# Optimization experiments

Measured on AMD Instinct MI355X. Metric: run time of the kernel, lower is better.

Reference implementation:

```python
import jax, jax.numpy as jnp
import numpy as np
from jax import lax

TAU = 1.0
SIGMAS = (1.0, 1.0, 1.0)
SIGMA_CUTOFF = 2.0
SCALE_FACTORS = (0.5, 1.0)
ITERATIONS = (4, 4)
EPS = 1e-6


def _grid(shape):
    # identity sampling grid in voxel coordinates, (3, D, H, W)
    return jnp.stack(jnp.meshgrid(*[jnp.arange(s, dtype=jnp.float32) for s in shape], indexing='ij'), axis=0)


def warp(vol, flow):
    # vol (B,C,D,H,W), flow (B,3,D,H,W) voxel-space displacements; trilinear, zeros padding
    g = _grid(vol.shape[2:])
    def one_b(v, f):
        coords = g + f  # (3,D,H,W)
        def one_c(ch):
            return jax.scipy.ndimage.map_coordinates(ch, [coords[0], coords[1], coords[2]], order=1, mode='constant', cval=0.0)
        return jax.vmap(one_c)(v)
    return jax.vmap(one_b)(vol, flow)


def gaussian_smooth(x, sigmas=SIGMAS):
    # separable depthwise Gaussian, kernel radius = ceil(sigma_cutoff * sigma)
    C = x.shape[1]
    for axis, sigma in enumerate(sigmas):
        r = int(np.ceil(SIGMA_CUTOFF * sigma))
        t = jnp.arange(-r, r + 1, dtype=x.dtype)
        k = jnp.exp(-0.5 * (t / sigma) ** 2)
        k = k / k.sum()
        kshape = [1, 1, 1, 1, 1]
        kshape[2 + axis] = k.size
        w = jnp.broadcast_to(k.reshape(kshape), (C, 1) + tuple(kshape[2:]))
        x = lax.conv_general_dilated(x, w, (1, 1, 1), 'SAME', feature_group_count=C,
                                     dimension_numbers=('NCDHW', 'OIDHW', 'NCDHW'))
    return x


def _gradient(x, axis):
    # np.gradient style: central diff interior, one-sided at edges, unit spacing
    lo = lax.slice_in_dim(x, 1, 2, axis=axis) - lax.slice_in_dim(x, 0, 1, axis=axis)
    mid = (lax.slice_in_dim(x, 2, None, axis=axis) - lax.slice_in_dim(x, 0, -2, axis=axis)) * 0.5
    hi = lax.slice_in_dim(x, -1, None, axis=axis) - lax.slice_in_dim(x, -2, -1, axis=axis)
    return jnp.concatenate([lo, mid, hi], axis=axis)


def demon_forces(moving, fixed):
    # active demons: gradient of (warped) moving image, (B,1,D,H,W) -> (B,3,D,H,W)
    m = moving[:, 0]
    grads = jnp.stack([_gradient(m, 1), _gradient(m, 2), _gradient(m, 3)], axis=1)
    diff = moving - fixed  # (B,1,D,H,W)
    denom = jnp.sum(grads ** 2, axis=1, keepdims=True) + diff ** 2
    return grads * diff / (denom + EPS)


def resize_tri(x, shape):
    return jax.image.resize(x, x.shape[:2] + tuple(shape), method='trilinear')


def match_vf(vf, shape):
    if tuple(vf.shape[2:]) == tuple(shape):
        return vf
    old = vf.shape[2:]
    out = resize_tri(vf, shape)
    scale = jnp.array([s1 / s2 for s1, s2 in zip(shape, old)], dtype=vf.dtype).reshape(1, 3, 1, 1, 1)
    return out * scale


def run_level(vf, img_s, mask_s, cond_s, iters):
    def body(i, carry):
        vf, _ = carry
        warped = warp(cond_s, vf)
        f = demon_forces(warped, img_s)
        vf = vf - TAU * (f * mask_s)
        vf = gaussian_smooth(vf)
        return (vf, warped)
    return lax.fori_loop(0, iters, body, (vf, jnp.zeros_like(cond_s)))


def conv3d(x, w, b=None):
    y = lax.conv_general_dilated(x, w, (1, 1, 1), 'SAME', dimension_numbers=('NCDHW', 'OIDHW', 'NCDHW'))
    return y if b is None else y + b[None, :, None, None, None]


def instance_norm(x, eps=1e-5):
    m = x.mean(axis=(2, 3, 4), keepdims=True)
    v = x.var(axis=(2, 3, 4), keepdims=True)
    return (x - m) * lax.rsqrt(v + eps)


def mish(x):
    return x * jnp.tanh(jax.nn.softplus(x))


def setup_inputs() -> dict:
    key = jax.random.key(0)
    ks = jax.random.split(key, 8)
    S = (1, 1, 96, 96, 96)
    image = jax.random.normal(ks[0], S, dtype=jnp.float32)
    conditional = jax.random.normal(ks[1], S, dtype=jnp.float32)
    mask = jnp.ones(S, dtype=jnp.float32)
    w1 = jax.random.normal(ks[2], (32, 5, 3, 3, 3), dtype=jnp.float32) * 0.05
    w2 = jax.random.normal(ks[3], (64, 32, 3, 3, 3), dtype=jnp.float32) * 0.05
    w3 = jax.random.normal(ks[4], (32, 64, 3, 3, 3), dtype=jnp.float32) * 0.05
    w4 = jax.random.normal(ks[5], (3, 32, 3, 3, 3), dtype=jnp.float32) * 0.05
    b4 = jnp.zeros((3,), dtype=jnp.float32)
    return {"image": image, "mask": mask, "conditional": conditional,
            "w1": w1, "w2": w2, "w3": w3, "w4": w4, "b4": b4}


def reference(image, mask, conditional, w1, w2, w3, w4, b4):
    full_shape = image.shape[2:]
    vf = None
    warped = None
    for sf, iters in zip(SCALE_FACTORS, ITERATIONS):
        shp = tuple(int(s * sf) for s in full_shape)
        img_s = resize_tri(image, shp)
        mask_s = jax.image.resize(mask, mask.shape[:2] + shp, method='nearest')
        cond_s = resize_tri(conditional, shp)
        if vf is None:
            vf = jnp.zeros((image.shape[0], 3) + shp, image.dtype)
        else:
            vf = match_vf(vf, shp)
        vf, warped = run_level(vf, img_s, mask_s, cond_s, iters)
    # correction network on full-resolution level outputs
    masked_image = image * mask
    stacked = jnp.concatenate([vf, masked_image, warped], axis=1)  # (B,5,D,H,W)
    h = mish(instance_norm(conv3d(stacked, w1)))
    h = mish(instance_norm(conv3d(h, w2)))
    h = mish(instance_norm(conv3d(h, w3)))
    corr = conv3d(h, w4, b4)
    cvf = gaussian_smooth(vf + corr)
    vf_full = match_vf(vf, full_shape)
    cvf_full = match_vf(cvf, full_shape)
    corrected_warped = warp(conditional, cvf_full)
    warped_full = warp(conditional, vf_full)
    return (corrected_warped, warped_full, cvf_full, vf_full)
```

## Files before the change

### kernel.cpp

```cpp
#include <hip/hip_runtime.h>
#include <math.h>

typedef unsigned short ushort_t;
typedef __attribute__((ext_vector_type(8))) short bf16x8;
typedef __attribute__((ext_vector_type(4))) float f32x4;

constexpr int V96 = 96 * 96 * 96;
constexpr int V48 = 48 * 48 * 48;
constexpr int V98 = 98 * 98 * 98;

__device__ __constant__ float GK[5] = {
    0.05448868454964294f, 0.24420134240717082f, 0.40261994608637245f,
    0.24420134240717082f, 0.05448868454964294f };

__device__ __forceinline__ float bf2f(ushort_t u) {
    return __uint_as_float(((unsigned)u) << 16);
}
__device__ __forceinline__ ushort_t f2bf(float f) {
    unsigned x = __float_as_uint(f);
    x += 0x7fffu + ((x >> 16) & 1u);
    return (ushort_t)(x >> 16);
}
__device__ __forceinline__ bool is_bf16(const unsigned* mrw) {
    return mrw[0] == 0x3F803F80u;
}
__device__ __forceinline__ float ld_in(const void* p, int i, bool bf) {
    return bf ? bf2f(((const ushort_t*)p)[i]) : ((const float*)p)[i];
}

constexpr size_t OFF_IMG32 = 0;
constexpr size_t OFF_MSK32 = OFF_IMG32 + V96;
constexpr size_t OFF_COND32 = OFF_MSK32 + V96;
constexpr size_t OFF_VF96 = OFF_COND32 + V96;
constexpr size_t OFF_WTS = OFF_VF96 + 3 * (size_t)V96;
constexpr size_t OFF_ST = OFF_WTS + 117760;
constexpr size_t OFF_PK1 = OFF_ST + 256;
constexpr size_t OFF_PK2 = OFF_PK1 + 3584;
constexpr size_t OFF_PK3 = OFF_PK2 + 27648;
constexpr size_t OFF_PK4 = OFF_PK3 + 27648;
constexpr size_t OFF_B = OFF_PK4 + 6912;
constexpr size_t BSZF = 32 * (size_t)V98 / 2;
constexpr size_t OFF_C = OFF_B + BSZF;
constexpr size_t CSZF = 64 * (size_t)V98;
constexpr size_t WS_FLOATS = OFF_C + CSZF / 2;

constexpr size_t WOB = 117504;

template<int S>
__device__ __forceinline__ void decomp(int r, int& z, int& y, int& x) {
    z = r / (S * S); int r2 = r - z * S * S; y = r2 / S; x = r2 - y * S;
}

__global__ void cvt_in_k(const void* __restrict__ in, float* __restrict__ out, int n,
                         const unsigned* __restrict__ mrw) {
    int i = blockIdx.x * 256 + threadIdx.x;
    if (i >= n) return;
    out[i] = ld_in(in, i, is_bf16(mrw));
}
__global__ void cvt3_k(const void* __restrict__ a, const void* __restrict__ b,
                       const void* __restrict__ c, float* __restrict__ oa,
                       float* __restrict__ ob, float* __restrict__ oc,
                       const unsigned* __restrict__ mrw) {
    int i = blockIdx.x * 256 + threadIdx.x;
    if (i >= V96) return;
    bool bf = is_bf16(mrw);
    oa[i] = ld_in(a, i, bf);
    ob[i] = ld_in(b, i, bf);
    oc[i] = ld_in(c, i, bf);
}
__global__ void store_out_k(const float* __restrict__ in, void* __restrict__ out,
                            size_t off, int n, const unsigned* __restrict__ mrw) {
    int i = blockIdx.x * 256 + threadIdx.x;
    if (i >= n) return;
    if (is_bf16(mrw)) ((ushort_t*)out)[off + i] = f2bf(in[i]);
    else              ((float*)out)[off + i] = in[i];
}
__global__ void add4_k(const float* __restrict__ a, const float* __restrict__ b,
                       float* __restrict__ o, int n4) {
    int i = blockIdx.x * 256 + threadIdx.x;
    if (i >= n4) return;
    float4 A = ((const float4*)a)[i], B = ((const float4*)b)[i];
    float4 O = {A.x + B.x, A.y + B.y, A.z + B.z, A.w + B.w};
    ((float4*)o)[i] = O;
}

template<int C>
__global__ void zero_pad_k(ushort_t* __restrict__ buf) {
    int v = blockIdx.x * 256 + threadIdx.x;
    if (v >= V98) return;
    int z = v / (98 * 98); int r = v - z * 98 * 98; int y = r / 98; int x = r - y * 98;
    if (z != 0 && z != 97 && y != 0 && y != 97 && x != 0 && x != 97) return;
    bf16x8 zv = {};
    bf16x8* p = (bf16x8*)(buf + (size_t)v * C);
#pragma unroll
    for (int c = 0; c < C / 8; ++c) p[c] = zv;
}

__global__ void pack1_k(const void* __restrict__ w, ushort_t* __restrict__ pk,
                        const unsigned* __restrict__ mrw) {
    int i = blockIdx.x * 256 + threadIdx.x;
    if (i >= 7168) return;
    bool bf = is_bf16(mrw);
    int j = i & 7, n = (i >> 3) & 15, ng = (i >> 7) & 1, tq = i >> 8;
    int co = ng * 16 + n;
    float v = (tq < 27 && j < 5) ? ld_in(w, (co * 5 + j) * 27 + tq, bf) : 0.f;
    pk[i] = f2bf(v);
}
__global__ void pack2_k(const void* __restrict__ w, ushort_t* __restrict__ pk,
                        const unsigned* __restrict__ mrw) {
    int i = blockIdx.x * 256 + threadIdx.x;
    if (i >= 55296) return;
    bool bf = is_bf16(mrw);
    int j = i & 7, n = (i >> 3) & 15, q = (i >> 7) & 3, ng = (i >> 9) & 3, t = i >> 11;
    int co = ng * 16 + n, ci = q * 8 + j;
    pk[i] = f2bf(ld_in(w, (co * 32 + ci) * 27 + t, bf));
}
__global__ void pack3_k(const void* __restrict__ w, ushort_t* __restrict__ pk,
                        const unsigned* __restrict__ mrw) {
    int i = blockIdx.x * 256 + threadIdx.x;
    if (i >= 55296) return;
    bool bf = is_bf16(mrw);
    int j = i & 7, n = (i >> 3) & 15, q = (i >> 7) & 3, ng = (i >> 9) & 1, kb = (i >> 10) & 1, t = i >> 11;
    int co = ng * 16 + n, ci = kb * 32 + q * 8 + j;
    pk[i] = f2bf(ld_in(w, (co * 64 + ci) * 27 + t, bf));
}
__global__ void pack4_k(const void* __restrict__ w, ushort_t* __restrict__ pk,
                        const unsigned* __restrict__ mrw) {
    int i = blockIdx.x * 256 + threadIdx.x;
    if (i >= 13824) return;
    bool bf = is_bf16(mrw);
    int j = i & 7, m = (i >> 3) & 15, q = (i >> 7) & 3, t = i >> 9;
    int ci = q * 8 + j;
    float v = (m < 3) ? ld_in(w, (m * 32 + ci) * 27 + t, bf) : 0.f;
    pk[i] = f2bf(v);
}

__device__ __forceinline__ int ds_wt(int i, float w[4]) {
    int j0 = 2 * i - 1;
    w[0] = 0.25f; w[1] = 0.75f; w[2] = 0.75f; w[3] = 0.25f;
    float s = 0.f;
#pragma unroll
    for (int t = 0; t < 4; ++t) { int j = j0 + t; if (j < 0 || j > 95) w[t] = 0.f; s += w[t]; }
    float inv = 1.f / s;
#pragma unroll
    for (int t = 0; t < 4; ++t) w[t] *= inv;
    return j0;
}

__global__ void down_tri_k(const float* __restrict__ in, float* __restrict__ out) {
    int idx = blockIdx.x * 256 + threadIdx.x;
    if (idx >= V48) return;
    int z, y, x; decomp<48>(idx, z, y, x);
    float wz[4], wy[4], wx[4];
    int z0 = ds_wt(z, wz), y0 = ds_wt(y, wy), x0 = ds_wt(x, wx);
    float acc = 0.f;
#pragma unroll
    for (int a = 0; a < 4; ++a) {
        int zz = z0 + a; zz = zz < 0 ? 0 : (zz > 95 ? 95 : zz);
#pragma unroll
        for (int b = 0; b < 4; ++b) {
            int yy = y0 + b; yy = yy < 0 ? 0 : (yy > 95 ? 95 : yy);
            float wzy = wz[a] * wy[b];
#pragma unroll
            for (int c = 0; c < 4; ++c) {
                int xx = x0 + c; xx = xx < 0 ? 0 : (xx > 95 ? 95 : xx);
                acc = fmaf(wzy * wx[c], in[(zz * 96 + yy) * 96 + xx], acc);
            }
        }
    }
    out[idx] = acc;
}

__global__ void down_near_k(const float* __restrict__ in, float* __restrict__ out) {
    int idx = blockIdx.x * 256 + threadIdx.x;
    if (idx >= V48) return;
    int z, y, x; decomp<48>(idx, z, y, x);
    out[idx] = in[((2 * z + 1) * 96 + (2 * y + 1)) * 96 + (2 * x + 1)];
}

__device__ __forceinline__ void up_c(int i, int& i0, float& t) {
    float s = 0.5f * (float)i - 0.25f;
    s = fminf(fmaxf(s, 0.f), 47.f);
    int ii = (int)s; if (ii > 46) ii = 46;
    i0 = ii; t = s - (float)ii;
}

__global__ void up_vf_k(const float* __restrict__ in, float* __restrict__ out) {
    int idx = blockIdx.x * 256 + threadIdx.x;
    if (idx >= 3 * V96) return;
    int c = idx / V96; int r = idx - c * V96;
    int z, y, x; decomp<96>(r, z, y, x);
    int z0, y0, x0; float tz, ty, tx;
    up_c(z, z0, tz); up_c(y, y0, ty); up_c(x, x0, tx);
    const float* p = in + (size_t)c * V48;
    float acc = 0.f;
#pragma unroll
    for (int a = 0; a < 2; ++a)
#pragma unroll
        for (int b = 0; b < 2; ++b)
#pragma unroll
            for (int d = 0; d < 2; ++d) {
                float w = (a ? tz : 1.f - tz) * (b ? ty : 1.f - ty) * (d ? tx : 1.f - tx);
                acc = fmaf(w, p[((z0 + a) * 48 + (y0 + b)) * 48 + (x0 + d)], acc);
            }
    out[idx] = 2.f * acc;
}

template<int S>
__global__ void warp_k(const float* __restrict__ vol, const float* __restrict__ flow,
                       float* __restrict__ out) {
    constexpr int S3 = S * S * S;
    int idx = blockIdx.x * 256 + threadIdx.x;
    if (idx >= S3) return;
    int z, y, x; decomp<S>(idx, z, y, x);
    float cz = (float)z + flow[idx];
    float cy = (float)y + flow[S3 + idx];
    float cx = (float)x + flow[2 * S3 + idx];
    float fz = floorf(cz), fy = floorf(cy), fx = floorf(cx);
    int iz = (int)fz, iy = (int)fy, ix = (int)fx;
    float tz = cz - fz, ty = cy - fy, tx = cx - fx;
    float acc = 0.f;
#pragma unroll
    for (int a = 0; a < 2; ++a)
#pragma unroll
        for (int b = 0; b < 2; ++b)
#pragma unroll
            for (int c = 0; c < 2; ++c) {
                int zz = iz + a, yy = iy + b, xx = ix + c;
                float w = (a ? tz : 1.f - tz) * (b ? ty : 1.f - ty) * (c ? tx : 1.f - tx);
                bool ok = ((unsigned)zz < (unsigned)S) && ((unsigned)yy < (unsigned)S) &&
                          ((unsigned)xx < (unsigned)S);
                float v = ok ? vol[(zz * S + yy) * S + xx] : 0.f;
                acc = fmaf(w, v, acc);
            }
    out[idx] = acc;
}

__global__ void warp_out_k(const float* __restrict__ vol, const float* __restrict__ flow,
                           void* __restrict__ out, size_t off,
                           const unsigned* __restrict__ mrw) {
    constexpr int S = 96, S3 = V96;
    int idx = blockIdx.x * 256 + threadIdx.x;
    if (idx >= S3) return;
    int z, y, x; decomp<S>(idx, z, y, x);
    float cz = (float)z + flow[idx];
    float cy = (float)y + flow[S3 + idx];
    float cx = (float)x + flow[2 * S3 + idx];
    float fz = floorf(cz), fy = floorf(cy), fx = floorf(cx);
    int iz = (int)fz, iy = (int)fy, ix = (int)fx;
    float tz = cz - fz, ty = cy - fy, tx = cx - fx;
    float acc = 0.f;
#pragma unroll
    for (int a = 0; a < 2; ++a)
#pragma unroll
        for (int b = 0; b < 2; ++b)
#pragma unroll
            for (int c = 0; c < 2; ++c) {
                int zz = iz + a, yy = iy + b, xx = ix + c;
                float w = (a ? tz : 1.f - tz) * (b ? ty : 1.f - ty) * (c ? tx : 1.f - tx);
                bool ok = ((unsigned)zz < (unsigned)S) && ((unsigned)yy < (unsigned)S) &&
                          ((unsigned)xx < (unsigned)S);
                float v = ok ? vol[(zz * S + yy) * S + xx] : 0.f;
                acc = fmaf(w, v, acc);
            }
    if (is_bf16(mrw)) ((ushort_t*)out)[off + idx] = f2bf(acc);
    else              ((float*)out)[off + idx] = acc;
}

template<int S>
__global__ void demon4_k(const float* __restrict__ wv, const float* __restrict__ fx_,
                         const float* __restrict__ msk, const float* __restrict__ vin,
                         float* __restrict__ vout) {
    constexpr int S3 = S * S * S;
    int u = blockIdx.x * 256 + threadIdx.x;
    if (u >= S3 / 4) return;
    int idx = u * 4;
    int z, y, x0; decomp<S>(idx, z, y, x0);
    float w[12];
    *(float4*)(w + 4) = *(const float4*)(wv + idx);
    if (x0 > 0) *(float4*)(w + 0) = *(const float4*)(wv + idx - 4);
    else { w[0] = w[1] = w[2] = w[3] = 0.f; }
    if (x0 < S - 4) *(float4*)(w + 8) = *(const float4*)(wv + idx + 4);
    else { w[8] = w[9] = w[10] = w[11] = 0.f; }
    float zp[4], zm[4], yp[4], ym[4];
    float sz = (z == 0 || z == S - 1) ? 1.f : 0.5f;
    float sy = (y == 0 || y == S - 1) ? 1.f : 0.5f;
    if (z > 0) *(float4*)zm = *(const float4*)(wv + idx - S * S);
    else { zm[0] = w[4]; zm[1] = w[5]; zm[2] = w[6]; zm[3] = w[7]; }
    if (z < S - 1) *(float4*)zp = *(const float4*)(wv + idx + S * S);
    else { zp[0] = w[4]; zp[1] = w[5]; zp[2] = w[6]; zp[3] = w[7]; }
    if (y > 0) *(float4*)ym = *(const float4*)(wv + idx - S);
    else { ym[0] = w[4]; ym[1] = w[5]; ym[2] = w[6]; ym[3] = w[7]; }
    if (y < S - 1) *(float4*)yp = *(const float4*)(wv + idx + S);
    else { yp[0] = w[4]; yp[1] = w[5]; yp[2] = w[6]; yp[3] = w[7]; }
    float fx4[4], mk4[4], v0[4], v1[4], v2[4], o0[4], o1[4], o2[4];
    *(float4*)fx4 = *(const float4*)(fx_ + idx);
    *(float4*)mk4 = *(const float4*)(msk + idx);
    *(float4*)v0 = *(const float4*)(vin + idx);
    *(float4*)v1 = *(const float4*)(vin + S3 + idx);
    *(float4*)v2 = *(const float4*)(vin + 2 * S3 + idx);
#pragma unroll
    for (int j = 0; j < 4; ++j) {
        int x = x0 + j;
        float m = w[4 + j];
        float gz = sz * (zp[j] - zm[j]);
        float gy = sy * (yp[j] - ym[j]);
        float gx = (x == 0) ? (w[j + 5] - w[j + 4])
                 : (x == S - 1) ? (w[j + 4] - w[j + 3])
                 : 0.5f * (w[j + 5] - w[j + 3]);
        float diff = m - fx4[j];
        float denom = gz * gz + gy * gy + gx * gx + diff * diff + 1e-6f;
        float r = diff / denom;
        float mk = mk4[j] * r;
        o0[j] = v0[j] - gz * mk;
        o1[j] = v1[j] - gy * mk;
        o2[j] = v2[j] - gx * mk;
    }
    *(float4*)(vout + idx) = *(float4*)o0;
    *(float4*)(vout + S3 + idx) = *(float4*)o1;
    *(float4*)(vout + 2 * S3 + idx) = *(float4*)o2;
}

template<int S, int ZC>
__global__ void smooth3d_k(const float* __restrict__ in, float* __restrict__ out) {
    constexpr int NZ = S / ZC;
    int idx = blockIdx.x * 256 + threadIdx.x;
    if (idx >= 3 * NZ * S * S) return;
    int x = idx % S;
    int y = (idx / S) % S;
    int zci = (idx / (S * S)) % NZ;
    int c = idx / (S * S * NZ);
    int z0 = zci * ZC;
    const float* p = in + (size_t)c * (S * S * S);
    float* o = out + (size_t)c * (S * S * S) + ((size_t)z0 * S + y) * S + x;
    float wx[5], wy[5];
    int xc[5], yc[5];
#pragma unroll
    for (int t = 0; t < 5; ++t) {
        int xx = x + t - 2, yy = y + t - 2;
        wx[t] = ((unsigned)xx < (unsigned)S) ? GK[t] : 0.f;
        xc[t] = xx < 0 ? 0 : (xx >= S ? S - 1 : xx);
        wy[t] = ((unsigned)yy < (unsigned)S) ? GK[t] : 0.f;
        yc[t] = yy < 0 ? 0 : (yy >= S ? S - 1 : yy);
    }
    float win[5] = {0.f, 0.f, 0.f, 0.f, 0.f};
#pragma unroll 1
    for (int k = 0; k < ZC + 4; ++k) {
        int zz = z0 - 2 + k;
        int zcl = zz < 0 ? 0 : (zz >= S ? S - 1 : zz);
        const float* ps = p + (size_t)zcl * S * S;
        float s = 0.f;
#pragma unroll
        for (int ty = 0; ty < 5; ++ty) {
            const float* pr = ps + yc[ty] * S;
            float rs = 0.f;
#pragma unroll
            for (int tx = 0; tx < 5; ++tx)
                rs = fmaf(wx[tx], pr[xc[tx]], rs);
            s = fmaf(wy[ty], rs, s);
        }
        s = ((unsigned)zz < (unsigned)S) ? s : 0.f;
        win[0] = win[1]; win[1] = win[2]; win[2] = win[3]; win[3] = win[4]; win[4] = s;
        if (k >= 4)
            o[(size_t)(k - 4) * S * S] =
                fmaf(GK[0], win[0], fmaf(GK[1], win[1], fmaf(GK[2], win[2],
                fmaf(GK[3], win[3], GK[4] * win[4]))));
    }
}

__global__ void build_st8_k(const float* __restrict__ vf, const float* __restrict__ img,
                            const float* __restrict__ msk, const float* __restrict__ wrp,
                            ushort_t* __restrict__ st8) {
    int idx = blockIdx.x * 256 + threadIdx.x;
    if (idx >= V96) return;
    int z, y, x; decomp<96>(idx, z, y, x);
    size_t pa = ((size_t)(z + 1) * 98 + (y + 1)) * 98 + (x + 1);
    union { bf16x8 v; ushort_t u[8]; } w;
    w.u[0] = f2bf(vf[idx]);
    w.u[1] = f2bf(vf[V96 + idx]);
    w.u[2] = f2bf(vf[2 * V96 + idx]);
    w.u[3] = f2bf(img[idx] * msk[idx]);
    w.u[4] = f2bf(wrp[idx]);
    w.u[5] = 0; w.u[6] = 0; w.u[7] = 0;
    *(bf16x8*)(st8 + pa * 8) = w.v;
}

__global__ __launch_bounds__(256) void conv1_mfma_k(const ushort_t* __restrict__ st8,
                                                    const ushort_t* __restrict__ pk,
                                                    ushort_t* __restrict__ out) {
    const int lane = threadIdx.x & 63;
    const int wv = threadIdx.x >> 6;
    const int ng = wv & 1;
    const int vs = wv >> 1;
    const int m = lane & 15;
    const int q = lane >> 4;
    const int x0 = blockIdx.x * 32 + vs * 16;
    const int y = blockIdx.y, z = blockIdx.z;
    f32x4 acc = {0.f, 0.f, 0.f, 0.f};
#pragma unroll
    for (int g = 0; g < 7; ++g) {
        int t = g * 4 + q;
        size_t pa = 0;
        if (t < 27) {
            int dz = t / 9, dy = (t / 3) % 3, dx = t % 3;
            pa = (((size_t)(z + dz) * 98) + (y + dy)) * 98 + (x0 + dx + m);
        }
        bf16x8 a = *(const bf16x8*)(st8 + pa * 8);
        bf16x8 b = *(const bf16x8*)(pk + (((size_t)t * 2 + ng) * 16 + m) * 8);
        acc = __builtin_amdgcn_mfma_f32_16x16x32_bf16(a, b, acc, 0, 0, 0);
    }
    const size_t pb = (((size_t)(z + 1) * 98) + (y + 1)) * 98 + (x0 + 1);
#pragma unroll
    for (int r = 0; r < 4; ++r) {
        int mm = q * 4 + r;
        out[(pb + mm) * 32 + ng * 16 + m] = f2bf(acc[r]);
    }
}

__global__ __launch_bounds__(256, 3) void conv2_lds_k(const ushort_t* __restrict__ in,
                                                      const ushort_t* __restrict__ pk,
                                                      ushort_t* __restrict__ out) {
    __shared__ bf16x8 sm[2160];
    const int tid = threadIdx.x;
    const int X0 = blockIdx.x * 16, Y0 = blockIdx.y * 4, Z0 = blockIdx.z * 2;
    for (int cid = tid; cid < 1728; cid += 256) {
        int r = cid / 72, c = cid - r * 72;
        int zz = r / 6, yy = r - zz * 6;
        int v = c >> 2, sub = c & 3;
        const bf16x8* gp = (const bf16x8*)(in +
            (((size_t)(Z0 + zz) * 98 + (Y0 + yy)) * 98 + X0 + v) * 32) + sub;
        sm[r * 90 + v * 5 + sub] = *gp;
    }
    __syncthreads();
    const int lane = tid & 63;
    const int wv = tid >> 6;
    const int w2 = wv >> 1;
    const int nh = wv & 1;
    const int m = lane & 15;
    const int q = lane >> 4;
    f32x4 acc[2][2][2] = {};
#pragma unroll 1
    for (int dx = 0; dx < 3; ++dx) {
        bf16x8 a[16];
#pragma unroll
        for (int zp = 0; zp < 4; ++zp)
#pragma unroll
            for (int iy = 0; iy < 4; ++iy)
                a[zp * 4 + iy] = sm[(zp * 6 + w2 * 2 + iy) * 90 + (dx + m) * 5 + q];
#pragma unroll
        for (int dz = 0; dz < 3; ++dz)
#pragma unroll
            for (int dy = 0; dy < 3; ++dy) {
                const int t = (dz * 3 + dy) * 3 + dx;
#pragma unroll
                for (int ngl = 0; ngl < 2; ++ngl) {
                    const int ng = nh * 2 + ngl;
                    bf16x8 b = *(const bf16x8*)(pk + ((((size_t)t * 4 + ng) * 4 + q) * 16 + m) * 8);
#pragma unroll
                    for (int z = 0; z < 2; ++z)
#pragma unroll
                        for (int yy = 0; yy < 2; ++yy)
                            acc[z][yy][ngl] = __builtin_amdgcn_mfma_f32_16x16x32_bf16(
                                a[(z + dz) * 4 + (yy + dy)], b, acc[z][yy][ngl], 0, 0, 0);
                }
            }
    }
#pragma unroll
    for (int z = 0; z < 2; ++z)
#pragma unroll
        for (int yy = 0; yy < 2; ++yy) {
            const size_t pb = (((size_t)(Z0 + z + 1) * 98) + (Y0 + w2 * 2 + yy + 1)) * 98 + (X0 + 1);
#pragma unroll
            for (int ngl = 0; ngl < 2; ++ngl) {
                const int ng = nh * 2 + ngl;
#pragma unroll
                for (int r = 0; r < 4; ++r) {
                    int mm = q * 4 + r;
                    out[(pb + mm) * 64 + ng * 16 + m] = f2bf(acc[z][yy][ngl][r]);
                }
            }
        }
}

__global__ __launch_bounds__(256, 4) void conv3_lds_k(const ushort_t* __restrict__ in,
                                                      const ushort_t* __restrict__ pk,
                                                      ushort_t* __restrict__ out) {
    __shared__ bf16x8 sm[2160];
    const int tid = threadIdx.x;
    const int X0 = blockIdx.x * 16, Y0 = blockIdx.y * 4, Z0 = blockIdx.z * 2;
    const int lane = tid & 63;
    const int wv = tid >> 6;
    const int w2 = wv >> 1;
    const int ng = wv & 1;
    const int m = lane & 15;
    const int q = lane >> 4;
    f32x4 acc[2][2] = {};
#pragma unroll 1
    for (int kb = 0; kb < 2; ++kb) {
        if (kb) __syncthreads();
        for (int cid = tid; cid < 1728; cid += 256) {
            int r = cid / 72, c = cid - r * 72;
            int zz = r / 6, yy = r - zz * 6;
            int v = c >> 2, sub = c & 3;
            const bf16x8* gp = (const bf16x8*)(in +
                (((size_t)(Z0 + zz) * 98 + (Y0 + yy)) * 98 + X0 + v) * 64 + kb * 32) + sub;
            sm[r * 90 + v * 5 + sub] = *gp;
        }
        __syncthreads();
#pragma unroll 1
        for (int dx = 0; dx < 3; ++dx) {
            bf16x8 a[16];
#pragma unroll
            for (int zp = 0; zp < 4; ++zp)
#pragma unroll
                for (int iy = 0; iy < 4; ++iy)
                    a[zp * 4 + iy] = sm[(zp * 6 + w2 * 2 + iy) * 90 + (dx + m) * 5 + q];
#pragma unroll
            for (int dz = 0; dz < 3; ++dz)
#pragma unroll
                for (int dy = 0; dy < 3; ++dy) {
                    const int t = (dz * 3 + dy) * 3 + dx;
                    bf16x8 b = *(const bf16x8*)(pk +
                        (((((size_t)t * 2 + kb) * 2 + ng) * 4 + q) * 16 + m) * 8);
#pragma unroll
                    for (int z = 0; z < 2; ++z)
#pragma unroll
                        for (int yy = 0; yy < 2; ++yy)
                            acc[z][yy] = __builtin_amdgcn_mfma_f32_16x16x32_bf16(
                                a[(z + dz) * 4 + (yy + dy)], b, acc[z][yy], 0, 0, 0);
                }
        }
    }
#pragma unroll
    for (int z = 0; z < 2; ++z)
#pragma unroll
        for (int yy = 0; yy < 2; ++yy) {
            const size_t pb = (((size_t)(Z0 + z + 1) * 98) + (Y0 + w2 * 2 + yy + 1)) * 98 + (X0 + 1);
#pragma unroll
            for (int r = 0; r < 4; ++r) {
                int mm = q * 4 + r;
                out[(pb + mm) * 32 + ng * 16 + m] = f2bf(acc[z][yy][r]);
            }
        }
}

__global__ __launch_bounds__(384) void conv4_mfma_k(const ushort_t* __restrict__ in,
                                                    const ushort_t* __restrict__ pk,
                                                    const float* __restrict__ bias,
                                                    float* __restrict__ out) {
    const int lane = threadIdx.x & 63;
    const int wv = threadIdx.x >> 6;
    const int n = lane & 15;
    const int q = lane >> 4;
    const int x0 = wv * 16;
    const int y = blockIdx.y, z = blockIdx.z;
    f32x4 acc = {0.f, 0.f, 0.f, 0.f};
    for (int dz = 0; dz < 3; ++dz)
        for (int dy = 0; dy < 3; ++dy)
#pragma unroll
            for (int dx = 0; dx < 3; ++dx) {
                const int t = (dz * 3 + dy) * 3 + dx;
                bf16x8 a = *(const bf16x8*)(pk + (((size_t)t * 4 + q) * 16 + n) * 8);
                bf16x8 b = *(const bf16x8*)(in +
                    ((((size_t)(z + dz) * 98) + (y + dy)) * 98 + (x0 + dx + n)) * 32 + q * 8);
                acc = __builtin_amdgcn_mfma_f32_16x16x32_bf16(a, b, acc, 0, 0, 0);
            }
    if (q == 0) {
        int ob = ((z * 96) + y) * 96 + x0 + n;
#pragma unroll
        for (int r = 0; r < 3; ++r)
            out[(size_t)r * V96 + ob] = acc[r] + bias[r];
    }
}

template<int C>
__global__ void stats_part_k(const ushort_t* __restrict__ buf, float* __restrict__ part) {
    constexpr size_t total = (size_t)V98 * C;
    const int tid = threadIdx.x;
    size_t chunk = (total + (size_t)gridDim.x * 256 - 1) / ((size_t)gridDim.x * 256) * 256;
    size_t i0 = (size_t)blockIdx.x * chunk;
    size_t i1 = i0 + chunk; if (i1 > total) i1 = total;
    float s = 0.f, qq = 0.f;
    for (size_t i = i0 + tid; i < i1; i += 256) {
        float v = bf2f(buf[i]); s += v; qq = fmaf(v, v, qq);
    }
    __shared__ float ls[256], lq[256];
    ls[tid] = s; lq[tid] = qq; __syncthreads();
    if (tid < C) {
        float S = 0.f, Q = 0.f;
        for (int j = tid; j < 256; j += C) { S += ls[j]; Q += lq[j]; }
        part[(size_t)blockIdx.x * 2 * C + tid] = S;
        part[(size_t)blockIdx.x * 2 * C + C + tid] = Q;
    }
}

template<int C>
__global__ void finalize_st_k(const float* __restrict__ part, float* __restrict__ st) {
    __shared__ float ls[256], lq[256];
    const int tid = threadIdx.x;
    const int c = tid % C;
    const int g = tid / C;
    constexpr int G = 256 / C;
    float S = 0.f, Q = 0.f;
    for (int b = g; b < 1024; b += G) {
        S += part[(size_t)b * 2 * C + c];
        Q += part[(size_t)b * 2 * C + C + c];
    }
    ls[tid] = S; lq[tid] = Q; __syncthreads();
    if (tid < C) {
        float Sa = 0.f, Qa = 0.f;
        for (int j = tid; j < 256; j += C) { Sa += ls[j]; Qa += lq[j]; }
        float mean = Sa * (1.f / 884736.f);
        float var = Qa * (1.f / 884736.f) - mean * mean;
        st[2 * tid] = mean;
        st[2 * tid + 1] = rsqrtf(var + 1e-5f);
    }
}

template<int C>
__global__ void inmish8_k(ushort_t* __restrict__ buf, const float* __restrict__ st) {
    size_t u = (size_t)blockIdx.x * 256 + threadIdx.x;
    if (u >= (size_t)C * V96 / 8) return;
    size_t i0 = u * 8;
    int v = (int)(i0 / C);
    int c0 = (int)(i0 % C);
    int z, y, x; decomp<96>(v, z, y, x);
    size_t pa = (((size_t)(z + 1) * 98 + (y + 1)) * 98 + (x + 1)) * C + c0;
    union { bf16x8 vv; ushort_t us[8]; } ld, stv;
    ld.vv = *(const bf16x8*)(buf + pa);
#pragma unroll
    for (int j = 0; j < 8; ++j) {
        int c = c0 + j;
        float mean = st[2 * c];
        float rstd = st[2 * c + 1];
        float val = (bf2f(ld.us[j]) - mean) * rstd;
        float vc = fminf(val, 30.f);
        float e = __builtin_amdgcn_exp2f(vc * 1.44269504088896f);
        float n = e * (e + 2.f);
        float r = n * __builtin_amdgcn_rcpf(n + 2.f);
        stv.us[j] = f2bf(val * r);
    }
    *(bf16x8*)(buf + pa) = stv.vv;
}

extern "C" void kernel_launch(void* const* d_in, const int* in_sizes, int n_in,
                              void* d_out, int out_size, void* d_ws, size_t ws_size,
                              hipStream_t stream) {
    const void* image_raw = d_in[0];
    const unsigned* mask_raw = (const unsigned*)d_in[1];
    const void* cond_raw = d_in[2];
    float* ws = (float*)d_ws;

    if (ws_size < WS_FLOATS * sizeof(float)) return;

    float* img32 = ws + OFF_IMG32;
    float* msk32 = ws + OFF_MSK32;
    float* cond32 = ws + OFF_COND32;
    float* vf96 = ws + OFF_VF96;
    float* wts = ws + OFF_WTS;
    float* st = ws + OFF_ST;
    ushort_t* pk1 = (ushort_t*)(ws + OFF_PK1);
    ushort_t* pk2 = (ushort_t*)(ws + OFF_PK2);
    ushort_t* pk3 = (ushort_t*)(ws + OFF_PK3);
    ushort_t* pk4 = (ushort_t*)(ws + OFF_PK4);
    float* Bf = ws + OFF_B;
    float* Cf = ws + OFF_C;

    float* t96a = Bf;
    float* l48 = Bf + 6 * (size_t)V96;
    float* img48 = l48;
    float* cond48 = l48 + V48;
    float* mask48 = l48 + 2 * (size_t)V48;
    float* warp48 = l48 + 3 * (size_t)V48;
    float* vf48   = l48 + 4 * (size_t)V48;
    float* t48a   = l48 + 7 * (size_t)V48;

    float* warped96 = Cf;
    ushort_t* st8 = (ushort_t*)(Cf + V96);
    float* corr     = Cf;
    float* cvtmp    = Cf + 3 * (size_t)V96;

    ushort_t* h1 = (ushort_t*)Bf;
    ushort_t* h2 = (ushort_t*)Cf;

    float* part = img32;

    auto g1 = [](int n) { return dim3((unsigned)((n + 255) / 256)); };

    cvt3_k<<<g1(V96), 256, 0, stream>>>(image_raw, (const void*)mask_raw, cond_raw,
                                        img32, msk32, cond32, mask_raw);
    cvt_in_k<<<1, 256, 0, stream>>>(d_in[7], wts + WOB, 3, mask_raw);
    pack1_k<<<g1(7168), 256, 0, stream>>>(d_in[3], pk1, mask_raw);
    pack2_k<<<g1(55296), 256, 0, stream>>>(d_in[4], pk2, mask_raw);
    pack3_k<<<g1(55296), 256, 0, stream>>>(d_in[5], pk3, mask_raw);
    pack4_k<<<g1(13824), 256, 0, stream>>>(d_in[6], pk4, mask_raw);

    down_tri_k<<<g1(V48), 256, 0, stream>>>(img32, img48);
    down_tri_k<<<g1(V48), 256, 0, stream>>>(cond32, cond48);
    down_near_k<<<g1(V48), 256, 0, stream>>>(msk32, mask48);
    hipMemsetAsync(vf48, 0, 3 * (size_t)V48 * sizeof(float), stream);

    for (int it = 0; it < 4; ++it) {
        warp_k<48><<<g1(V48), 256, 0, stream>>>(cond48, vf48, warp48);
        demon4_k<48><<<g1(V48 / 4), 256, 0, stream>>>(warp48, img48, mask48, vf48, t48a);
        smooth3d_k<48, 6><<<g1(3 * 8 * 48 * 48), 256, 0, stream>>>(t48a, vf48);
    }

    up_vf_k<<<g1(3 * V96), 256, 0, stream>>>(vf48, vf96);

    for (int it = 0; it < 4; ++it) {
        warp_k<96><<<g1(V96), 256, 0, stream>>>(cond32, vf96, warped96);
        demon4_k<96><<<g1(V96 / 4), 256, 0, stream>>>(warped96, img32, msk32, vf96, t96a);
        smooth3d_k<96, 12><<<g1(3 * 8 * 96 * 96), 256, 0, stream>>>(t96a, vf96);
    }

    zero_pad_k<32><<<g1(V98), 256, 0, stream>>>((ushort_t*)Bf);
    zero_pad_k<8><<<g1(V98), 256, 0, stream>>>(st8);
    build_st8_k<<<g1(V96), 256, 0, stream>>>(vf96, img32, msk32, warped96, st8);

    conv1_mfma_k<<<dim3(3, 96, 96), 256, 0, stream>>>(st8, pk1, h1);
    stats_part_k<32><<<1024, 256, 0, stream>>>(h1, part);
    finalize_st_k<32><<<1, 256, 0, stream>>>(part, st + 0);
    inmish8_k<32><<<g1(32 * V96 / 8), 256, 0, stream>>>(h1, st + 0);

    zero_pad_k<64><<<g1(V98), 256, 0, stream>>>((ushort_t*)Cf);

    conv2_lds_k<<<dim3(6, 24, 48), 256, 0, stream>>>(h1, pk2, h2);
    stats_part_k<64><<<1024, 256, 0, stream>>>(h2, part);
    finalize_st_k<64><<<1, 256, 0, stream>>>(part, st + 64);
    inmish8_k<64><<<g1(64 * V96 / 8), 256, 0, stream>>>(h2, st + 64);

    conv3_lds_k<<<dim3(6, 24, 48), 256, 0, stream>>>(h2, pk3, h1);
    stats_part_k<32><<<1024, 256, 0, stream>>>(h1, part);
    finalize_st_k<32><<<1, 256, 0, stream>>>(part, st + 192);
    inmish8_k<32><<<g1(32 * V96 / 8), 256, 0, stream>>>(h1, st + 192);

    conv4_mfma_k<<<dim3(1, 96, 96), 384, 0, stream>>>(h1, pk4, wts + WOB, corr);

    add4_k<<<g1(3 * V96 / 4), 256, 0, stream>>>(vf96, corr, cvtmp, 3 * V96 / 4);
    smooth3d_k<96, 12><<<g1(3 * 8 * 96 * 96), 256, 0, stream>>>(cvtmp, Cf);

    store_out_k<<<g1(3 * V96), 256, 0, stream>>>(Cf, d_out, 2 * (size_t)V96, 3 * V96, mask_raw);
    warp_out_k<<<g1(V96), 256, 0, stream>>>(cond32, Cf, d_out, 0, mask_raw);
    warp_out_k<<<g1(V96), 256, 0, stream>>>(cond32, vf96, d_out, (size_t)V96, mask_raw);
    store_out_k<<<g1(3 * V96), 256, 0, stream>>>(vf96, d_out, 5 * (size_t)V96, 3 * V96, mask_raw);
}
```

Baseline: 1.432 ms.

## Fuse instance-norm statistics into conv epilogues and residual add into conv4

Each conv kernel now reduces per-channel sums and sums of squares from its accumulators via lane shuffles and LDS, then writes per-block partials. A new per-channel finalize kernel replaces the separate stats pass that re-read the whole bf16 activation buffer. Conv4 also adds vf directly in its store, removing the add4 kernel and a full-volume round trip. In exchange the partial buffers grow and the stats are taken from fp32 accumulators instead of rounded bf16 values, which shifts the numerics slightly.

```diff
diff --git a/kernel.cpp b/kernel.cpp
--- a/kernel.cpp
+++ b/kernel.cpp
@@ -74,14 +74,6 @@
     if (i >= n) return;
     if (is_bf16(mrw)) ((ushort_t*)out)[off + i] = f2bf(in[i]);
     else              ((float*)out)[off + i] = in[i];
-}
-__global__ void add4_k(const float* __restrict__ a, const float* __restrict__ b,
-                       float* __restrict__ o, int n4) {
-    int i = blockIdx.x * 256 + threadIdx.x;
-    if (i >= n4) return;
-    float4 A = ((const float4*)a)[i], B = ((const float4*)b)[i];
-    float4 O = {A.x + B.x, A.y + B.y, A.z + B.z, A.w + B.w};
-    ((float4*)o)[i] = O;
 }
 
 template<int C>
@@ -387,9 +379,11 @@
 
 __global__ __launch_bounds__(256) void conv1_mfma_k(const ushort_t* __restrict__ st8,
                                                     const ushort_t* __restrict__ pk,
-                                                    ushort_t* __restrict__ out) {
-    const int lane = threadIdx.x & 63;
-    const int wv = threadIdx.x >> 6;
+                                                    ushort_t* __restrict__ out,
+                                                    float* __restrict__ part) {
+    const int tid = threadIdx.x;
+    const int lane = tid & 63;
+    const int wv = tid >> 6;
     const int ng = wv & 1;
     const int vs = wv >> 1;
     const int m = lane & 15;
@@ -415,11 +409,27 @@
         int mm = q * 4 + r;
         out[(pb + mm) * 32 + ng * 16 + m] = f2bf(acc[r]);
     }
+    float s = acc[0] + acc[1] + acc[2] + acc[3];
+    float sq = acc[0] * acc[0] + acc[1] * acc[1] + acc[2] * acc[2] + acc[3] * acc[3];
+    s += __shfl_xor(s, 16);  s += __shfl_xor(s, 32);
+    sq += __shfl_xor(sq, 16); sq += __shfl_xor(sq, 32);
+    __shared__ float red[4][2][16];
+    if (q == 0) { red[wv][0][m] = s; red[wv][1][m] = sq; }
+    __syncthreads();
+    if (tid < 64) {
+        int which = tid >> 5;
+        int c = tid & 31;
+        int cg = c >> 4, cm = c & 15;
+        float v = red[cg][which][cm] + red[cg + 2][which][cm];
+        size_t row = ((size_t)blockIdx.z * 96 + blockIdx.y) * 3 + blockIdx.x;
+        part[row * 64 + tid] = v;
+    }
 }
 
 __global__ __launch_bounds__(256, 3) void conv2_lds_k(const ushort_t* __restrict__ in,
                                                       const ushort_t* __restrict__ pk,
-                                                      ushort_t* __restrict__ out) {
+                                                      ushort_t* __restrict__ out,
+                                                      float* __restrict__ part) {
     __shared__ bf16x8 sm[2160];
     const int tid = threadIdx.x;
     const int X0 = blockIdx.x * 16, Y0 = blockIdx.y * 4, Z0 = blockIdx.z * 2;
@@ -480,11 +490,40 @@
                 }
             }
         }
+    float s0 = 0.f, q0 = 0.f, s1 = 0.f, q1 = 0.f;
+#pragma unroll
+    for (int z = 0; z < 2; ++z)
+#pragma unroll
+        for (int yy = 0; yy < 2; ++yy)
+#pragma unroll
+            for (int r = 0; r < 4; ++r) {
+                float v0 = acc[z][yy][0][r]; s0 += v0; q0 = fmaf(v0, v0, q0);
+                float v1 = acc[z][yy][1][r]; s1 += v1; q1 = fmaf(v1, v1, q1);
+            }
+    s0 += __shfl_xor(s0, 16); s0 += __shfl_xor(s0, 32);
+    q0 += __shfl_xor(q0, 16); q0 += __shfl_xor(q0, 32);
+    s1 += __shfl_xor(s1, 16); s1 += __shfl_xor(s1, 32);
+    q1 += __shfl_xor(q1, 16); q1 += __shfl_xor(q1, 32);
+    __shared__ float red[4][2][2][16];
+    if (q == 0) {
+        red[wv][0][0][m] = s0; red[wv][0][1][m] = q0;
+        red[wv][1][0][m] = s1; red[wv][1][1][m] = q1;
+    }
+    __syncthreads();
+    if (tid < 128) {
+        int which = tid >> 6;
+        int c = tid & 63;
+        int cnh = (c >> 5) & 1, cngl = (c >> 4) & 1, cm = c & 15;
+        float v = red[cnh][cngl][which][cm] + red[2 + cnh][cngl][which][cm];
+        size_t row = ((size_t)blockIdx.z * 24 + blockIdx.y) * 6 + blockIdx.x;
+        part[row * 128 + tid] = v;
+    }
 }
 
 __global__ __launch_bounds__(256, 4) void conv3_lds_k(const ushort_t* __restrict__ in,
                                                       const ushort_t* __restrict__ pk,
-                                                      ushort_t* __restrict__ out) {
+                                                      ushort_t* __restrict__ out,
+                                                      float* __restrict__ part) {
     __shared__ bf16x8 sm[2160];
     const int tid = threadIdx.x;
     const int X0 = blockIdx.x * 16, Y0 = blockIdx.y * 4, Z0 = blockIdx.z * 2;
@@ -542,11 +581,34 @@
                 out[(pb + mm) * 32 + ng * 16 + m] = f2bf(acc[z][yy][r]);
             }
         }
+    float s = 0.f, sq = 0.f;
+#pragma unroll
+    for (int z = 0; z < 2; ++z)
+#pragma unroll
+        for (int yy = 0; yy < 2; ++yy)
+#pragma unroll
+            for (int r = 0; r < 4; ++r) {
+                float v = acc[z][yy][r]; s += v; sq = fmaf(v, v, sq);
+            }
+    s += __shfl_xor(s, 16);  s += __shfl_xor(s, 32);
+    sq += __shfl_xor(sq, 16); sq += __shfl_xor(sq, 32);
+    __shared__ float red[4][2][16];
+    if (q == 0) { red[wv][0][m] = s; red[wv][1][m] = sq; }
+    __syncthreads();
+    if (tid < 64) {
+        int which = tid >> 5;
+        int c = tid & 31;
+        int cg = c >> 4, cm = c & 15;
+        float v = red[cg][which][cm] + red[cg + 2][which][cm];
+        size_t row = ((size_t)blockIdx.z * 24 + blockIdx.y) * 6 + blockIdx.x;
+        part[row * 64 + tid] = v;
+    }
 }
 
 __global__ __launch_bounds__(384) void conv4_mfma_k(const ushort_t* __restrict__ in,
                                                     const ushort_t* __restrict__ pk,
                                                     const float* __restrict__ bias,
+                                                    const float* __restrict__ vf,
                                                     float* __restrict__ out) {
     const int lane = threadIdx.x & 63;
     const int wv = threadIdx.x >> 6;
@@ -555,7 +617,9 @@
     const int x0 = wv * 16;
     const int y = blockIdx.y, z = blockIdx.z;
     f32x4 acc = {0.f, 0.f, 0.f, 0.f};
+#pragma unroll 1
     for (int dz = 0; dz < 3; ++dz)
+#pragma unroll
         for (int dy = 0; dy < 3; ++dy)
 #pragma unroll
             for (int dx = 0; dx < 3; ++dx) {
@@ -569,51 +633,31 @@
         int ob = ((z * 96) + y) * 96 + x0 + n;
 #pragma unroll
         for (int r = 0; r < 3; ++r)
-            out[(size_t)r * V96 + ob] = acc[r] + bias[r];
+            out[(size_t)r * V96 + ob] = acc[r] + bias[r] + vf[(size_t)r * V96 + ob];
     }
 }
 
 template<int C>
-__global__ void stats_part_k(const ushort_t* __restrict__ buf, float* __restrict__ part) {
-    constexpr size_t total = (size_t)V98 * C;
+__global__ void finalize2_k(const float* __restrict__ part, int nrows,
+                            float* __restrict__ st) {
+    const int c = blockIdx.x;
     const int tid = threadIdx.x;
-    size_t chunk = (total + (size_t)gridDim.x * 256 - 1) / ((size_t)gridDim.x * 256) * 256;
-    size_t i0 = (size_t)blockIdx.x * chunk;
-    size_t i1 = i0 + chunk; if (i1 > total) i1 = total;
-    float s = 0.f, qq = 0.f;
-    for (size_t i = i0 + tid; i < i1; i += 256) {
-        float v = bf2f(buf[i]); s += v; qq = fmaf(v, v, qq);
+    float s = 0.f, q = 0.f;
+    for (int r = tid; r < nrows; r += 256) {
+        s += part[(size_t)r * 2 * C + c];
+        q += part[(size_t)r * 2 * C + C + c];
     }
     __shared__ float ls[256], lq[256];
-    ls[tid] = s; lq[tid] = qq; __syncthreads();
-    if (tid < C) {
-        float S = 0.f, Q = 0.f;
-        for (int j = tid; j < 256; j += C) { S += ls[j]; Q += lq[j]; }
-        part[(size_t)blockIdx.x * 2 * C + tid] = S;
-        part[(size_t)blockIdx.x * 2 * C + C + tid] = Q;
-    }
-}
-
-template<int C>
-__global__ void finalize_st_k(const float* __restrict__ part, float* __restrict__ st) {
-    __shared__ float ls[256], lq[256];
-    const int tid = threadIdx.x;
-    const int c = tid % C;
-    const int g = tid / C;
-    constexpr int G = 256 / C;
-    float S = 0.f, Q = 0.f;
-    for (int b = g; b < 1024; b += G) {
-        S += part[(size_t)b * 2 * C + c];
-        Q += part[(size_t)b * 2 * C + C + c];
-    }
-    ls[tid] = S; lq[tid] = Q; __syncthreads();
-    if (tid < C) {
-        float Sa = 0.f, Qa = 0.f;
-        for (int j = tid; j < 256; j += C) { Sa += ls[j]; Qa += lq[j]; }
-        float mean = Sa * (1.f / 884736.f);
-        float var = Qa * (1.f / 884736.f) - mean * mean;
-        st[2 * tid] = mean;
-        st[2 * tid + 1] = rsqrtf(var + 1e-5f);
+    ls[tid] = s; lq[tid] = q; __syncthreads();
+    for (int off = 128; off; off >>= 1) {
+        if (tid < off) { ls[tid] += ls[tid + off]; lq[tid] += lq[tid + off]; }
+        __syncthreads();
+    }
+    if (tid == 0) {
+        float mean = ls[0] * (1.f / 884736.f);
+        float var = lq[0] * (1.f / 884736.f) - mean * mean;
+        st[2 * c] = mean;
+        st[2 * c + 1] = rsqrtf(var + 1e-5f);
     }
 }
 
@@ -677,7 +721,6 @@
 
     float* warped96 = Cf;
     ushort_t* st8 = (ushort_t*)(Cf + V96);
-    float* corr     = Cf;
     float* cvtmp    = Cf + 3 * (size_t)V96;
 
     ushort_t* h1 = (ushort_t*)Bf;
@@ -718,26 +761,22 @@
     zero_pad_k<8><<<g1(V98), 256, 0, stream>>>(st8);
     build_st8_k<<<g1(V96), 256, 0, stream>>>(vf96, img32, msk32, warped96, st8);
 
-    conv1_mfma_k<<<dim3(3, 96, 96), 256, 0, stream>>>(st8, pk1, h1);
-    stats_part_k<32><<<1024, 256, 0, stream>>>(h1, part);
-    finalize_st_k<32><<<1, 256, 0, stream>>>(part, st + 0);
+    conv1_mfma_k<<<dim3(3, 96, 96), 256, 0, stream>>>(st8, pk1, h1, part);
+    finalize2_k<32><<<32, 256, 0, stream>>>(part, 27648, st + 0);
     inmish8_k<32><<<g1(32 * V96 / 8), 256, 0, stream>>>(h1, st + 0);
 
     zero_pad_k<64><<<g1(V98), 256, 0, stream>>>((ushort_t*)Cf);
 
-    conv2_lds_k<<<dim3(6, 24, 48), 256, 0, stream>>>(h1, pk2, h2);
-    stats_part_k<64><<<1024, 256, 0, stream>>>(h2, part);
-    finalize_st_k<64><<<1, 256, 0, stream>>>(part, st + 64);
+    conv2_lds_k<<<dim3(6, 24, 48), 256, 0, stream>>>(h1, pk2, h2, part);
+    finalize2_k<64><<<64, 256, 0, stream>>>(part, 6912, st + 64);
     inmish8_k<64><<<g1(64 * V96 / 8), 256, 0, stream>>>(h2, st + 64);
 
-    conv3_lds_k<<<dim3(6, 24, 48), 256, 0, stream>>>(h2, pk3, h1);
-    stats_part_k<32><<<1024, 256, 0, stream>>>(h1, part);
-    finalize_st_k<32><<<1, 256, 0, stream>>>(part, st + 192);
+    conv3_lds_k<<<dim3(6, 24, 48), 256, 0, stream>>>(h2, pk3, h1, part);
+    finalize2_k<32><<<32, 256, 0, stream>>>(part, 6912, st + 192);
     inmish8_k<32><<<g1(32 * V96 / 8), 256, 0, stream>>>(h1, st + 192);
 
-    conv4_mfma_k<<<dim3(1, 96, 96), 384, 0, stream>>>(h1, pk4, wts + WOB, corr);
-
-    add4_k<<<g1(3 * V96 / 4), 256, 0, stream>>>(vf96, corr, cvtmp, 3 * V96 / 4);
+    conv4_mfma_k<<<dim3(1, 96, 96), 384, 0, stream>>>(h1, pk4, wts + WOB, vf96, cvtmp);
+
     smooth3d_k<96, 12><<<g1(3 * 8 * 96 * 96), 256, 0, stream>>>(cvtmp, Cf);
 
     store_out_k<<<g1(3 * V96), 256, 0, stream>>>(Cf, d_out, 2 * (size_t)V96, 3 * V96, mask_raw);
```

New measurement: 1.241 ms. 13.3% less time.
